# Kernel optimization log

Measured on AMD Instinct MI355X. Metric: run time of the kernel, lower is better.

## Reference

```python
import jax, jax.numpy as jnp
import numpy as np

NUM_HEADS = 8
FREQ_RATIO = 0.5


def _resize_bilinear(img, out_h, out_w):
    """Bilinear resize of last two dims, matching torch interpolate align_corners=False."""
    in_h, in_w = img.shape[-2], img.shape[-1]

    def idx(in_size, out_size):
        src = jnp.maximum((jnp.arange(out_size, dtype=jnp.float32) + 0.5) * (in_size / out_size) - 0.5, 0.0)
        i0 = jnp.floor(src).astype(jnp.int32)
        i1 = jnp.minimum(i0 + 1, in_size - 1)
        w = src - i0.astype(jnp.float32)
        return i0, i1, w

    r0, r1, wr = idx(in_h, out_h)
    img = img[..., r0, :] * (1.0 - wr)[:, None] + img[..., r1, :] * wr[:, None]
    c0, c1, wc = idx(in_w, out_w)
    img = img[..., c0] * (1.0 - wc) + img[..., c1] * wc
    return img


def setup_inputs() -> dict:
    key = jax.random.key(0)
    ks = jax.random.split(key, 6)
    B, T, J, C = 4, 256, 17, 512
    H = NUM_HEADS
    x = jax.random.normal(ks[0], (B, T, J, C), dtype=jnp.float32)
    att_map = jax.random.uniform(ks[1], (B, H, J, T, T), dtype=jnp.float32)
    weight = jax.random.uniform(ks[2], (1,), dtype=jnp.float32)
    w_qkv = jax.random.normal(ks[3], (C, 3 * C), dtype=jnp.float32) * 0.02
    w_proj = jax.random.normal(ks[4], (C, C), dtype=jnp.float32) * 0.02
    b_proj = jnp.zeros((C,), dtype=jnp.float32)
    freq_gate = jnp.ones((1,), dtype=jnp.float32)
    return {"x": x, "att_map": att_map, "weight": weight, "w_qkv": w_qkv,
            "w_proj": w_proj, "b_proj": b_proj, "freq_gate": freq_gate}


def reference(x, att_map, weight, w_qkv, w_proj, b_proj, freq_gate):
    B, T, J, C = x.shape
    H = NUM_HEADS
    d = C // H
    scale = d ** (-0.5)

    qkv = (x @ w_qkv).reshape(B, T, J, 3, H, d)
    qkv = jnp.transpose(qkv, (3, 0, 4, 2, 1, 5))  # [3,B,H,J,T,d]
    q, k, v = qkv[0], qkv[1], qkv[2]

    # time-domain attention over T, per (B,H,J)
    attn_time = jax.nn.softmax(jnp.einsum('bhjtd,bhjsd->bhjts', q, k) * scale, axis=-1)

    # frequency-domain attention
    qf = jnp.fft.rfft(q, axis=3)
    kf = jnp.fft.rfft(k, axis=3)
    F = qf.shape[3]                      # T//2 + 1
    keep = max(1, int(F * FREQ_RATIO))
    qf = qf[:, :, :, :keep]
    kf = kf[:, :, :, :keep]
    af = jnp.einsum('bhjfd,bhjgd->bhjfg', qf, jnp.conj(kf)) * scale  # complex [B,H,J,keep,keep]
    # torch combines softmax(real) + 1j*softmax(imag); only the real part survives
    af_real = jax.nn.softmax(af.real, axis=-1)
    af_real = jnp.pad(af_real, ((0, 0), (0, 0), (0, 0), (0, F - keep), (0, 0)))  # zero-pad rows to F
    attn_freq = _resize_bilinear(af_real, T, T)  # [B,H,J,T,T]

    gate = jax.nn.sigmoid(freq_gate)  # broadcastable scalar
    attn_self = gate * attn_freq + (1.0 - gate) * attn_time
    attn = weight * attn_self + (1.0 - weight) * att_map

    out = jnp.einsum('bhjts,bhjsd->bhjtd', attn, v)        # [B,H,J,T,d]
    out = jnp.transpose(out, (0, 3, 2, 1, 4)).reshape(B, T, J, C)
    return out @ w_proj + b_proj
```

## Files before the change

kernel.cpp:

```cpp
#include <hip/hip_runtime.h>
#include <hip/hip_bf16.h>


#define SCALE 0.125f
#define LSTR 72

typedef __attribute__((ext_vector_type(4))) float f32x4;
typedef __attribute__((ext_vector_type(8))) short bf16x8;
typedef __attribute__((ext_vector_type(8))) unsigned short u16x8;

__device__ __forceinline__ float bf2f(unsigned short u) {
  return __uint_as_float(((unsigned int)u) << 16);
}
__device__ __forceinline__ unsigned short f2bf(float f) {
  unsigned int u = __float_as_uint(f);
  u += 0x7FFFu + ((u >> 16) & 1u);
  return (unsigned short)(u >> 16);
}

__global__ __launch_bounds__(256) void conv_x(
    const float* __restrict__ x, unsigned short* __restrict__ xh,
    unsigned short* __restrict__ xl) {
  const size_t i = ((size_t)blockIdx.x * 256 + threadIdx.x) * 8;
  float4 a = *(const float4*)(x + i);
  float4 b = *(const float4*)(x + i + 4);
  float vv[8] = {a.x, a.y, a.z, a.w, b.x, b.y, b.z, b.w};
  u16x8 hi, lo;
#pragma unroll
  for (int e = 0; e < 8; ++e) {
    unsigned short h = f2bf(vv[e]);
    hi[e] = h;
    lo[e] = f2bf(vv[e] - bf2f(h));
  }
  *(u16x8*)&xh[i] = hi;
  *(u16x8*)&xl[i] = lo;
}

__global__ __launch_bounds__(256) void conv_wT(
    const float* __restrict__ w, unsigned short* __restrict__ th,
    unsigned short* __restrict__ tl, int N) {
  __shared__ float T[64][65];
  const int tid = threadIdx.x;
  const int nt = blockIdx.x * 64, kt = blockIdx.y * 64;
  for (int i = tid; i < 4096; i += 256) {
    const int r = i >> 6, c = i & 63;
    T[r][c] = w[(size_t)(kt + r) * N + nt + c];
  }
  __syncthreads();
  for (int i = tid; i < 4096; i += 256) {
    const int rn = i >> 6, ck = i & 63;
    const float v = T[ck][rn];
    const unsigned short h = f2bf(v);
    const size_t o = (size_t)(nt + rn) * 512 + kt + ck;
    th[o] = h;
    tl[o] = f2bf(v - bf2f(h));
  }
}

__global__ __launch_bounds__(256, 2) void qkv_gemm(
    const unsigned short* __restrict__ xh, const unsigned short* __restrict__ xl,
    const unsigned short* __restrict__ wh, const unsigned short* __restrict__ wl,
    float* __restrict__ q, float* __restrict__ k, float* __restrict__ v) {
  __shared__ __attribute__((aligned(16))) unsigned short Wt[2][128 * LSTR];
  __shared__ __attribute__((aligned(16))) unsigned short Xt[2][128 * LSTR];

  const int tid = threadIdx.x;
  const int bx = blockIdx.x, by = blockIdx.y;
  const int wid = tid >> 6, lane = tid & 63;
  const int lr = lane & 15, lg = lane >> 4;
  const int wr = wid >> 1, wc = wid & 1;
  const int srow = tid >> 3, skg = tid & 7;

  const unsigned short* xhp = xh + (size_t)(by * 128 + srow) * 512 + skg * 8;
  const unsigned short* xlp = xl + (size_t)(by * 128 + srow) * 512 + skg * 8;
  const unsigned short* whp = wh + (size_t)(bx * 128 + srow) * 512 + skg * 8;
  const unsigned short* wlp = wl + (size_t)(bx * 128 + srow) * 512 + skg * 8;

  u16x8 rxh[4], rxl[4], rwh[4], rwl[4];
  auto loadk = [&](int k0) {
#pragma unroll
    for (int it = 0; it < 4; ++it) {
      const size_t o = (size_t)(32 * it) * 512 + k0;
      rxh[it] = *(const u16x8*)(xhp + o);
      rxl[it] = *(const u16x8*)(xlp + o);
      rwh[it] = *(const u16x8*)(whp + o);
      rwl[it] = *(const u16x8*)(wlp + o);
    }
  };

  f32x4 acc[4][4];
#pragma unroll
  for (int nt = 0; nt < 4; ++nt)
#pragma unroll
    for (int mt = 0; mt < 4; ++mt) acc[nt][mt] = (f32x4){0.f, 0.f, 0.f, 0.f};

  loadk(0);
  for (int s = 0; s < 8; ++s) {
    if (s) __syncthreads();
#pragma unroll
    for (int it = 0; it < 4; ++it) {
      const int base = (srow + 32 * it) * LSTR + skg * 8;
      *(u16x8*)&Xt[0][base] = rxh[it];
      *(u16x8*)&Xt[1][base] = rxl[it];
      *(u16x8*)&Wt[0][base] = rwh[it];
      *(u16x8*)&Wt[1][base] = rwl[it];
    }
    __syncthreads();
    if (s < 7) loadk((s + 1) * 64);
#pragma unroll
    for (int kh = 0; kh < 2; ++kh) {
      const int kbase = kh * 32 + lg * 8;
      bf16x8 Ah[4], Al[4], Bh[4], Bl[4];
#pragma unroll
      for (int nt = 0; nt < 4; ++nt) {
        const int n = wr * 64 + nt * 16 + lr;
        Ah[nt] = *(bf16x8*)&Wt[0][n * LSTR + kbase];
        Al[nt] = *(bf16x8*)&Wt[1][n * LSTR + kbase];
      }
#pragma unroll
      for (int mt = 0; mt < 4; ++mt) {
        const int m = wc * 64 + mt * 16 + lr;
        Bh[mt] = *(bf16x8*)&Xt[0][m * LSTR + kbase];
        Bl[mt] = *(bf16x8*)&Xt[1][m * LSTR + kbase];
      }
#pragma unroll
      for (int nt = 0; nt < 4; ++nt)
#pragma unroll
        for (int mt = 0; mt < 4; ++mt) {
          acc[nt][mt] = __builtin_amdgcn_mfma_f32_16x16x32_bf16(Ah[nt], Bh[mt], acc[nt][mt], 0, 0, 0);
          acc[nt][mt] = __builtin_amdgcn_mfma_f32_16x16x32_bf16(Ah[nt], Bl[mt], acc[nt][mt], 0, 0, 0);
          acc[nt][mt] = __builtin_amdgcn_mfma_f32_16x16x32_bf16(Al[nt], Bh[mt], acc[nt][mt], 0, 0, 0);
        }
    }
  }

#pragma unroll
  for (int mt = 0; mt < 4; ++mt) {
    const int m = by * 128 + wc * 64 + mt * 16 + lr;
    const int jj = m % 17;
    const int bt = m / 17;
    const int t = bt & 255;
    const int b = bt >> 8;
#pragma unroll
    for (int nt = 0; nt < 4; ++nt) {
      const int c = bx * 128 + wr * 64 + nt * 16 + lg * 4;
      const int qi = c >> 9;
      const int h = (c >> 6) & 7;
      const int dd = c & 63;
      float* dst = (qi == 0) ? q : (qi == 1) ? k : v;
      *(float4*)&dst[((size_t)((b * 8 + h) * 17 + jj)) * 16384 + t * 64 + dd] =
          make_float4(acc[nt][mt][0], acc[nt][mt][1], acc[nt][mt][2], acc[nt][mt][3]);
    }
  }
}

__global__ __launch_bounds__(256) void freq_kernel(
    const float* __restrict__ qg, const float* __restrict__ kg,
    float* __restrict__ af_out) {
  __shared__ __attribute__((aligned(16))) unsigned short qT[2][64 * 256];
  __shared__ __attribute__((aligned(16))) unsigned short QF[4][64 * 64];
  __shared__ __attribute__((aligned(16))) unsigned short KF[4][64 * 64];

  const int tid = threadIdx.x;
  const int head = blockIdx.x;
  const int w = tid >> 6, lane = tid & 63;
  const int lr = lane & 15, lg = lane >> 4;
  const int f0 = w << 4;

  bf16x8 Ech[8], Ecl[8], Esh[8], Esl[8];
  {
    const int f = f0 + lr;
#pragma unroll
    for (int kb = 0; kb < 8; ++kb) {
      bf16x8 ch, cl, sh, sl;
#pragma unroll
      for (int i = 0; i < 8; ++i) {
        int t = kb * 32 + lg * 8 + i;
        int idx = (f * t) & 255;
        float s, c;
        __sincosf((float)idx * 0.02454369260617026f, &s, &c);
        unsigned short chh = f2bf(c);
        unsigned short shh = f2bf(s);
        ch[i] = (short)chh;
        cl[i] = (short)f2bf(c - bf2f(chh));
        sh[i] = (short)shh;
        sl[i] = (short)f2bf(s - bf2f(shh));
      }
      Ech[kb] = ch; Ecl[kb] = cl; Esh[kb] = sh; Esl[kb] = sl;
    }
  }

  for (int pass = 0; pass < 2; ++pass) {
    const float* src = pass ? kg : qg;
    __syncthreads();
    const float4* s4 = (const float4*)(src + head * 16384);
    for (int i = tid; i < 4096; i += 256) {
      int t = i >> 4, dq = i & 15;
      float4 v4 = s4[i];
      float vv[4] = {v4.x, v4.y, v4.z, v4.w};
#pragma unroll
      for (int c = 0; c < 4; ++c) {
        int d = dq * 4 + c;
        unsigned short hi = f2bf(vv[c]);
        unsigned short lo = f2bf(vv[c] - bf2f(hi));
        int byo = d * 512 + ((t * 2) ^ ((d & 31) << 4));
        *(unsigned short*)((char*)qT[0] + byo) = hi;
        *(unsigned short*)((char*)qT[1] + byo) = lo;
      }
    }
    __syncthreads();

    f32x4 ar[4], ai[4];
#pragma unroll
    for (int nt = 0; nt < 4; ++nt) {
      ar[nt] = (f32x4){0.f, 0.f, 0.f, 0.f};
      ai[nt] = (f32x4){0.f, 0.f, 0.f, 0.f};
    }
#pragma unroll
    for (int kb = 0; kb < 8; ++kb) {
#pragma unroll
      for (int nt = 0; nt < 4; ++nt) {
        const int d = nt * 16 + lr;
        const int byo = d * 512 + ((kb * 64 + lg * 16) ^ ((d & 31) << 4));
        bf16x8 bh = *(bf16x8*)((char*)qT[0] + byo);
        bf16x8 bl = *(bf16x8*)((char*)qT[1] + byo);
        ar[nt] = __builtin_amdgcn_mfma_f32_16x16x32_bf16(Ech[kb], bh, ar[nt], 0, 0, 0);
        ar[nt] = __builtin_amdgcn_mfma_f32_16x16x32_bf16(Ech[kb], bl, ar[nt], 0, 0, 0);
        ar[nt] = __builtin_amdgcn_mfma_f32_16x16x32_bf16(Ecl[kb], bh, ar[nt], 0, 0, 0);
        ai[nt] = __builtin_amdgcn_mfma_f32_16x16x32_bf16(Esh[kb], bh, ai[nt], 0, 0, 0);
        ai[nt] = __builtin_amdgcn_mfma_f32_16x16x32_bf16(Esh[kb], bl, ai[nt], 0, 0, 0);
        ai[nt] = __builtin_amdgcn_mfma_f32_16x16x32_bf16(Esl[kb], bh, ai[nt], 0, 0, 0);
      }
    }
    unsigned short(*DST)[64 * 64] = pass ? KF : QF;
#pragma unroll
    for (int nt = 0; nt < 4; ++nt) {
#pragma unroll
      for (int j = 0; j < 4; ++j) {
        const int f = f0 + lg * 4 + j;
        const int d = nt * 16 + lr;
        const int byo = f * 128 + ((d * 2) ^ ((f & 7) << 4));
        float vr = ar[nt][j], vi = ai[nt][j];
        unsigned short rh = f2bf(vr);
        unsigned short ih = f2bf(vi);
        *(unsigned short*)((char*)DST[0] + byo) = rh;
        *(unsigned short*)((char*)DST[1] + byo) = f2bf(vr - bf2f(rh));
        *(unsigned short*)((char*)DST[2] + byo) = ih;
        *(unsigned short*)((char*)DST[3] + byo) = f2bf(vi - bf2f(ih));
      }
    }
  }
  __syncthreads();

  f32x4 acc[4];
#pragma unroll
  for (int nt = 0; nt < 4; ++nt) acc[nt] = (f32x4){0.f, 0.f, 0.f, 0.f};
#pragma unroll
  for (int kb = 0; kb < 2; ++kb) {
    const int fA = f0 + lr;
    const int abyo = fA * 128 + ((kb * 64 + lg * 16) ^ ((fA & 7) << 4));
    bf16x8 arh = *(bf16x8*)((char*)QF[0] + abyo);
    bf16x8 arl = *(bf16x8*)((char*)QF[1] + abyo);
    bf16x8 aih = *(bf16x8*)((char*)QF[2] + abyo);
    bf16x8 ail = *(bf16x8*)((char*)QF[3] + abyo);
#pragma unroll
    for (int nt = 0; nt < 4; ++nt) {
      const int g = nt * 16 + lr;
      const int bbyo = g * 128 + ((kb * 64 + lg * 16) ^ ((g & 7) << 4));
      bf16x8 brh = *(bf16x8*)((char*)KF[0] + bbyo);
      bf16x8 brl = *(bf16x8*)((char*)KF[1] + bbyo);
      bf16x8 bih = *(bf16x8*)((char*)KF[2] + bbyo);
      bf16x8 bil = *(bf16x8*)((char*)KF[3] + bbyo);
      acc[nt] = __builtin_amdgcn_mfma_f32_16x16x32_bf16(arh, brh, acc[nt], 0, 0, 0);
      acc[nt] = __builtin_amdgcn_mfma_f32_16x16x32_bf16(arh, brl, acc[nt], 0, 0, 0);
      acc[nt] = __builtin_amdgcn_mfma_f32_16x16x32_bf16(arl, brh, acc[nt], 0, 0, 0);
      acc[nt] = __builtin_amdgcn_mfma_f32_16x16x32_bf16(aih, bih, acc[nt], 0, 0, 0);
      acc[nt] = __builtin_amdgcn_mfma_f32_16x16x32_bf16(aih, bil, acc[nt], 0, 0, 0);
      acc[nt] = __builtin_amdgcn_mfma_f32_16x16x32_bf16(ail, bih, acc[nt], 0, 0, 0);
    }
  }

  float* outh = af_out + head * 4096;
#pragma unroll
  for (int j = 0; j < 4; ++j) {
    float m = fmaxf(fmaxf(acc[0][j], acc[1][j]), fmaxf(acc[2][j], acc[3][j]));
#pragma unroll
    for (int mask = 1; mask < 16; mask <<= 1) m = fmaxf(m, __shfl_xor(m, mask));
    float e[4];
    float rs = 0.f;
#pragma unroll
    for (int nt = 0; nt < 4; ++nt) {
      e[nt] = __expf((acc[nt][j] - m) * SCALE);
      rs += e[nt];
    }
#pragma unroll
    for (int mask = 1; mask < 16; mask <<= 1) rs += __shfl_xor(rs, mask);
    const float inv = 1.0f / rs;
    const int f = f0 + lg * 4 + j;
#pragma unroll
    for (int nt = 0; nt < 4; ++nt) outh[f * 64 + nt * 16 + lr] = e[nt] * inv;
  }
}

__global__ __launch_bounds__(256) void attn_kernel(
    const float* __restrict__ qg, const float* __restrict__ kg,
    const float* __restrict__ vg, const float* __restrict__ af,
    const float* __restrict__ att_map, const float* __restrict__ weight,
    const float* __restrict__ fgate, float* __restrict__ out_perm) {
  __shared__ unsigned short Ks[256 * 64];
  __shared__ unsigned short Vt[64 * 256];
  __shared__ unsigned short afl[64 * 66];
  __shared__ unsigned short Psc[4][16 * 40];

  const int tid = threadIdx.x;
  const int t0 = blockIdx.x << 6;
  const int head = blockIdx.y;
  const int jj = head % 17;
  const int hb = head / 17;
  const int h = hb & 7;
  const int b = hb >> 3;

  const float4* ksrc = (const float4*)(kg + head * 16384);
  const float4* vsrc = (const float4*)(vg + head * 16384);
  for (int i = tid; i < 4096; i += 256) {
    int s = i >> 4, dq = i & 15;
    float4 kf = ksrc[i];
    ushort4 k4 = make_ushort4(f2bf(kf.x), f2bf(kf.y), f2bf(kf.z), f2bf(kf.w));
    int koff = s * 128 + ((dq * 8) ^ ((s & 7) << 4));
    *(ushort4*)((char*)Ks + koff) = k4;
    float4 vf = vsrc[i];
    float vv[4] = {vf.x, vf.y, vf.z, vf.w};
#pragma unroll
    for (int c = 0; c < 4; ++c) {
      int d = dq * 4 + c;
      int voff = d * 512 + ((s * 2) ^ ((d & 7) << 4));
      *(unsigned short*)((char*)Vt + voff) = f2bf(vv[c]);
    }
  }
  const float4* asrc = (const float4*)(af + head * 4096);
  for (int i = tid; i < 1024; i += 256) {
    float4 a4 = asrc[i];
    int f = i >> 4, gq = (i & 15) << 2;
    ushort4 a4b = make_ushort4(f2bf(a4.x), f2bf(a4.y), f2bf(a4.z), f2bf(a4.w));
    *(ushort4*)&afl[f * 66 + gq] = a4b;
  }
  __syncthreads();

  const int w = tid >> 6, lane = tid & 63;
  const int lr = lane & 15, lg = lane >> 4;
  const int tw = t0 + w * 16;

  bf16x8 aq[2];
  {
    const float* qrow = qg + head * 16384 + (tw + lr) * 64 + lg * 8;
#pragma unroll
    for (int kc = 0; kc < 2; ++kc) {
      float4 q0 = *(const float4*)(qrow + kc * 32);
      float4 q1 = *(const float4*)(qrow + kc * 32 + 4);
      bf16x8 a;
      a[0] = (short)f2bf(q0.x); a[1] = (short)f2bf(q0.y);
      a[2] = (short)f2bf(q0.z); a[3] = (short)f2bf(q0.w);
      a[4] = (short)f2bf(q1.x); a[5] = (short)f2bf(q1.y);
      a[6] = (short)f2bf(q1.z); a[7] = (short)f2bf(q1.w);
      aq[kc] = a;
    }
  }

  f32x4 S[16];
#pragma unroll
  for (int nt = 0; nt < 16; ++nt) {
    f32x4 accv = {0.f, 0.f, 0.f, 0.f};
#pragma unroll
    for (int kc = 0; kc < 2; ++kc) {
      int srow = nt * 16 + lr;
      int d0 = kc * 32 + lg * 8;
      int off = srow * 128 + ((d0 * 2) ^ ((srow & 7) << 4));
      bf16x8 bk = *(bf16x8*)((char*)Ks + off);
      accv = __builtin_amdgcn_mfma_f32_16x16x32_bf16(aq[kc], bk, accv, 0, 0, 0);
    }
    S[nt] = accv;
  }

  float inv[4], mrow[4];
#pragma unroll
  for (int j = 0; j < 4; ++j) {
    float m = -1e30f;
#pragma unroll
    for (int nt = 0; nt < 16; ++nt) m = fmaxf(m, S[nt][j]);
#pragma unroll
    for (int mask = 1; mask < 16; mask <<= 1) m = fmaxf(m, __shfl_xor(m, mask));
    mrow[j] = m;
  }
#pragma unroll
  for (int j = 0; j < 4; ++j) {
    float rs = 0.f;
#pragma unroll
    for (int nt = 0; nt < 16; ++nt) {
      float e = __expf((S[nt][j] - mrow[j]) * SCALE);
      S[nt][j] = e;
      rs += e;
    }
#pragma unroll
    for (int mask = 1; mask < 16; mask <<= 1) rs += __shfl_xor(rs, mask);
    inv[j] = 1.0f / rs;
  }

  {
    const float wv = weight[0];
    const float gate = 1.0f / (1.0f + __expf(-fgate[0]));
    const float* amh = att_map + (size_t)head * 65536;
#pragma unroll
    for (int j = 0; j < 4; ++j) {
      const int t = tw + lg * 4 + j;
      float srcf = fmaxf((t + 0.5f) * (129.0f / 256.0f) - 0.5f, 0.0f);
      int f0r = (int)srcf;
      float wf = srcf - (float)f0r;
      int f1r = f0r + 1;
      if (f1r > 128) f1r = 128;
      const bool v0 = (f0r < 64), v1 = (f1r < 64);
#pragma unroll
      for (int nt = 0; nt < 16; ++nt) {
        const int s = nt * 16 + lr;
        float am = amh[t * 256 + s];
        float srcg = fmaxf((s + 0.5f) * 0.25f - 0.5f, 0.0f);
        int g0 = (int)srcg;
        float wc = srcg - (float)g0;
        int g1 = g0 + 1;
        if (g1 > 63) g1 = 63;
        float fr = 0.f;
        if (v0)
          fr += (1.0f - wf) *
                (bf2f(afl[f0r * 66 + g0]) * (1.0f - wc) + bf2f(afl[f0r * 66 + g1]) * wc);
        if (v1)
          fr += wf *
                (bf2f(afl[f1r * 66 + g0]) * (1.0f - wc) + bf2f(afl[f1r * 66 + g1]) * wc);
        float pt = S[nt][j] * inv[j];
        S[nt][j] = wv * (gate * fr + (1.0f - gate) * pt) + (1.0f - wv) * am;
      }
    }
  }

  f32x4 O[4];
#pragma unroll
  for (int dt = 0; dt < 4; ++dt) O[dt] = (f32x4){0.f, 0.f, 0.f, 0.f};
  unsigned short* psc = Psc[w];
#pragma unroll
  for (int sb = 0; sb < 8; ++sb) {
#pragma unroll
    for (int half = 0; half < 2; ++half) {
      const int nt = sb * 2 + half;
#pragma unroll
      for (int j = 0; j < 4; ++j) {
        psc[(lg * 4 + j) * 40 + half * 16 + lr] = f2bf(S[nt][j]);
      }
    }
    bf16x8 pa = *(bf16x8*)&psc[lr * 40 + lg * 8];
#pragma unroll
    for (int dt = 0; dt < 4; ++dt) {
      int d = dt * 16 + lr;
      int s0 = sb * 32 + lg * 8;
      int off = d * 512 + ((s0 * 2) ^ ((d & 7) << 4));
      bf16x8 bv = *(bf16x8*)((char*)Vt + off);
      O[dt] = __builtin_amdgcn_mfma_f32_16x16x32_bf16(pa, bv, O[dt], 0, 0, 0);
    }
  }

#pragma unroll
  for (int j = 0; j < 4; ++j) {
    const int t = tw + lg * 4 + j;
    float* orow = out_perm + ((size_t)((b * 256 + t) * 17 + jj)) * 512 + h * 64;
#pragma unroll
    for (int dt = 0; dt < 4; ++dt) {
      orow[dt * 16 + lr] = O[dt][j];
    }
  }
}

__global__ __launch_bounds__(256, 2) void proj_gemm(
    const float* __restrict__ A,
    const unsigned short* __restrict__ wh, const unsigned short* __restrict__ wl,
    const float* __restrict__ bias, float* __restrict__ out) {
  __shared__ __attribute__((aligned(16))) unsigned short Wt[2][128 * LSTR];
  __shared__ __attribute__((aligned(16))) unsigned short Xt[2][128 * LSTR];

  const int tid = threadIdx.x;
  const int bx = blockIdx.x, by = blockIdx.y;
  const int wid = tid >> 6, lane = tid & 63;
  const int lr = lane & 15, lg = lane >> 4;
  const int wr = wid >> 1, wc = wid & 1;
  const int srow = tid >> 3, skg = tid & 7;

  const float* ap = A + (size_t)(by * 128 + srow) * 512 + skg * 8;
  const unsigned short* whp = wh + (size_t)(bx * 128 + srow) * 512 + skg * 8;
  const unsigned short* wlp = wl + (size_t)(bx * 128 + srow) * 512 + skg * 8;

  float4 rA[4][2];
  u16x8 rwh[4], rwl[4];
  auto loadk = [&](int k0) {
#pragma unroll
    for (int it = 0; it < 4; ++it) {
      const size_t o = (size_t)(32 * it) * 512 + k0;
      rA[it][0] = *(const float4*)(ap + o);
      rA[it][1] = *(const float4*)(ap + o + 4);
      rwh[it] = *(const u16x8*)(whp + o);
      rwl[it] = *(const u16x8*)(wlp + o);
    }
  };

  f32x4 acc[4][4];
#pragma unroll
  for (int nt = 0; nt < 4; ++nt)
#pragma unroll
    for (int mt = 0; mt < 4; ++mt) acc[nt][mt] = (f32x4){0.f, 0.f, 0.f, 0.f};

  loadk(0);
  for (int s = 0; s < 8; ++s) {
    if (s) __syncthreads();
#pragma unroll
    for (int it = 0; it < 4; ++it) {
      const int base = (srow + 32 * it) * LSTR + skg * 8;
      float vv[8] = {rA[it][0].x, rA[it][0].y, rA[it][0].z, rA[it][0].w,
                     rA[it][1].x, rA[it][1].y, rA[it][1].z, rA[it][1].w};
      u16x8 hi, lo;
#pragma unroll
      for (int e = 0; e < 8; ++e) {
        unsigned short h = f2bf(vv[e]);
        hi[e] = h;
        lo[e] = f2bf(vv[e] - bf2f(h));
      }
      *(u16x8*)&Xt[0][base] = hi;
      *(u16x8*)&Xt[1][base] = lo;
      *(u16x8*)&Wt[0][base] = rwh[it];
      *(u16x8*)&Wt[1][base] = rwl[it];
    }
    __syncthreads();
    if (s < 7) loadk((s + 1) * 64);
#pragma unroll
    for (int kh = 0; kh < 2; ++kh) {
      const int kbase = kh * 32 + lg * 8;
      bf16x8 Ah[4], Al[4], Bh[4], Bl[4];
#pragma unroll
      for (int nt = 0; nt < 4; ++nt) {
        const int n = wr * 64 + nt * 16 + lr;
        Ah[nt] = *(bf16x8*)&Wt[0][n * LSTR + kbase];
        Al[nt] = *(bf16x8*)&Wt[1][n * LSTR + kbase];
      }
#pragma unroll
      for (int mt = 0; mt < 4; ++mt) {
        const int m = wc * 64 + mt * 16 + lr;
        Bh[mt] = *(bf16x8*)&Xt[0][m * LSTR + kbase];
        Bl[mt] = *(bf16x8*)&Xt[1][m * LSTR + kbase];
      }
#pragma unroll
      for (int nt = 0; nt < 4; ++nt)
#pragma unroll
        for (int mt = 0; mt < 4; ++mt) {
          acc[nt][mt] = __builtin_amdgcn_mfma_f32_16x16x32_bf16(Ah[nt], Bh[mt], acc[nt][mt], 0, 0, 0);
          acc[nt][mt] = __builtin_amdgcn_mfma_f32_16x16x32_bf16(Ah[nt], Bl[mt], acc[nt][mt], 0, 0, 0);
          acc[nt][mt] = __builtin_amdgcn_mfma_f32_16x16x32_bf16(Al[nt], Bh[mt], acc[nt][mt], 0, 0, 0);
        }
    }
  }

#pragma unroll
  for (int mt = 0; mt < 4; ++mt) {
    const int m = by * 128 + wc * 64 + mt * 16 + lr;
#pragma unroll
    for (int nt = 0; nt < 4; ++nt) {
      const int n = bx * 128 + wr * 64 + nt * 16 + lg * 4;
      float4 bi = *(const float4*)&bias[n];
      *(float4*)&out[(size_t)m * 512 + n] =
          make_float4(acc[nt][mt][0] + bi.x, acc[nt][mt][1] + bi.y,
                      acc[nt][mt][2] + bi.z, acc[nt][mt][3] + bi.w);
    }
  }
}

extern "C" void kernel_launch(void* const* d_in, const int* in_sizes, int n_in,
                              void* d_out, int out_size, void* d_ws, size_t ws_size,
                              hipStream_t stream) {
  (void)in_sizes; (void)n_in; (void)out_size; (void)ws_size;
  const float* x = (const float*)d_in[0];
  const float* att_map = (const float*)d_in[1];
  const float* weight = (const float*)d_in[2];
  const float* w_qkv = (const float*)d_in[3];
  const float* w_proj = (const float*)d_in[4];
  const float* b_proj = (const float*)d_in[5];
  const float* fgate = (const float*)d_in[6];
  float* out = (float*)d_out;

  char* ws = (char*)d_ws;
  const size_t HB = 35651584;
  const size_t AF = 8912896;
  float* qb = (float*)(ws);
  float* kb = (float*)(ws + HB);
  float* vb = (float*)(ws + 2 * HB);
  float* af = (float*)(ws + 3 * HB);
  char* base = ws + 3 * HB + AF;
  unsigned short* xh = (unsigned short*)(base);
  unsigned short* xl = (unsigned short*)(base + 17825792);
  float* out_perm = (float*)(base);
  unsigned short* wqh = (unsigned short*)(base + 35651584);
  unsigned short* wql = (unsigned short*)(base + 35651584 + 1572864);
  unsigned short* wph = (unsigned short*)(base + 35651584 + 2 * 1572864);
  unsigned short* wpl = (unsigned short*)(base + 35651584 + 2 * 1572864 + 524288);

  conv_x<<<4352, 256, 0, stream>>>(x, xh, xl);
  conv_wT<<<dim3(24, 8), 256, 0, stream>>>(w_qkv, wqh, wql, 1536);
  conv_wT<<<dim3(8, 8), 256, 0, stream>>>(w_proj, wph, wpl, 512);
  qkv_gemm<<<dim3(12, 136), 256, 0, stream>>>(xh, xl, wqh, wql, qb, kb, vb);
  freq_kernel<<<544, 256, 0, stream>>>(qb, kb, af);
  attn_kernel<<<dim3(4, 544), 256, 0, stream>>>(qb, kb, vb, af, att_map, weight,
                                                fgate, out_perm);
  proj_gemm<<<dim3(4, 136), 256, 0, stream>>>(out_perm, wph, wpl, b_proj, out);
}
```

Baseline: 412.7 us.

## Store q/k/v as split bf16 in the GEMM epilogue and process one head per attention block

The QKV GEMM epilogue now writes q and k as hi/lo bf16 pairs and v as hi-only bf16 instead of fp32. The frequency kernel also writes its softmax output in bf16. This cuts intermediate write and read traffic and removes the repeated fp32-to-bf16 conversion in the consumers. The attention kernel now runs one block per head and loops over four 16-row tiles per wave, so K, V and the frequency map are staged into shared memory once per head instead of four times, and the next q rows are prefetched. The trade-offs are fewer blocks (544) with more serial work each, and bf16 rounding of the frequency map before it reaches global memory.

```diff
diff --git a/kernel.cpp b/kernel.cpp
--- a/kernel.cpp
+++ b/kernel.cpp
@@ -60,7 +60,9 @@
 __global__ __launch_bounds__(256, 2) void qkv_gemm(
     const unsigned short* __restrict__ xh, const unsigned short* __restrict__ xl,
     const unsigned short* __restrict__ wh, const unsigned short* __restrict__ wl,
-    float* __restrict__ q, float* __restrict__ k, float* __restrict__ v) {
+    unsigned short* __restrict__ qh, unsigned short* __restrict__ ql,
+    unsigned short* __restrict__ kh, unsigned short* __restrict__ kl,
+    unsigned short* __restrict__ vh) {
   __shared__ __attribute__((aligned(16))) unsigned short Wt[2][128 * LSTR];
   __shared__ __attribute__((aligned(16))) unsigned short Xt[2][128 * LSTR];
 
@@ -108,8 +110,8 @@
     __syncthreads();
     if (s < 7) loadk((s + 1) * 64);
 #pragma unroll
-    for (int kh = 0; kh < 2; ++kh) {
-      const int kbase = kh * 32 + lg * 8;
+    for (int kh2 = 0; kh2 < 2; ++kh2) {
+      const int kbase = kh2 * 32 + lg * 8;
       bf16x8 Ah[4], Al[4], Bh[4], Bl[4];
 #pragma unroll
       for (int nt = 0; nt < 4; ++nt) {
@@ -147,16 +149,28 @@
       const int qi = c >> 9;
       const int h = (c >> 6) & 7;
       const int dd = c & 63;
-      float* dst = (qi == 0) ? q : (qi == 1) ? k : v;
-      *(float4*)&dst[((size_t)((b * 8 + h) * 17 + jj)) * 16384 + t * 64 + dd] =
-          make_float4(acc[nt][mt][0], acc[nt][mt][1], acc[nt][mt][2], acc[nt][mt][3]);
+      const size_t base = ((size_t)((b * 8 + h) * 17 + jj)) * 16384 + t * 64 + dd;
+      float a0 = acc[nt][mt][0], a1 = acc[nt][mt][1], a2 = acc[nt][mt][2],
+            a3 = acc[nt][mt][3];
+      ushort4 hi4 = make_ushort4(f2bf(a0), f2bf(a1), f2bf(a2), f2bf(a3));
+      if (qi == 2) {
+        *(ushort4*)&vh[base] = hi4;
+      } else {
+        ushort4 lo4 = make_ushort4(f2bf(a0 - bf2f(hi4.x)), f2bf(a1 - bf2f(hi4.y)),
+                                   f2bf(a2 - bf2f(hi4.z)), f2bf(a3 - bf2f(hi4.w)));
+        unsigned short* dh = qi ? kh : qh;
+        unsigned short* dl = qi ? kl : ql;
+        *(ushort4*)&dh[base] = hi4;
+        *(ushort4*)&dl[base] = lo4;
+      }
     }
   }
 }
 
 __global__ __launch_bounds__(256) void freq_kernel(
-    const float* __restrict__ qg, const float* __restrict__ kg,
-    float* __restrict__ af_out) {
+    const unsigned short* __restrict__ qhp, const unsigned short* __restrict__ qlp,
+    const unsigned short* __restrict__ khp, const unsigned short* __restrict__ klp,
+    unsigned short* __restrict__ af_out) {
   __shared__ __attribute__((aligned(16))) unsigned short qT[2][64 * 256];
   __shared__ __attribute__((aligned(16))) unsigned short QF[4][64 * 64];
   __shared__ __attribute__((aligned(16))) unsigned short KF[4][64 * 64];
@@ -191,21 +205,21 @@
   }
 
   for (int pass = 0; pass < 2; ++pass) {
-    const float* src = pass ? kg : qg;
+    const unsigned short* sh_ = (pass ? khp : qhp) + head * 16384;
+    const unsigned short* sl_ = (pass ? klp : qlp) + head * 16384;
     __syncthreads();
-    const float4* s4 = (const float4*)(src + head * 16384);
     for (int i = tid; i < 4096; i += 256) {
       int t = i >> 4, dq = i & 15;
-      float4 v4 = s4[i];
-      float vv[4] = {v4.x, v4.y, v4.z, v4.w};
+      ushort4 hv = *(const ushort4*)&sh_[t * 64 + dq * 4];
+      ushort4 lv = *(const ushort4*)&sl_[t * 64 + dq * 4];
+      unsigned short hvv[4] = {hv.x, hv.y, hv.z, hv.w};
+      unsigned short lvv[4] = {lv.x, lv.y, lv.z, lv.w};
 #pragma unroll
       for (int c = 0; c < 4; ++c) {
         int d = dq * 4 + c;
-        unsigned short hi = f2bf(vv[c]);
-        unsigned short lo = f2bf(vv[c] - bf2f(hi));
         int byo = d * 512 + ((t * 2) ^ ((d & 31) << 4));
-        *(unsigned short*)((char*)qT[0] + byo) = hi;
-        *(unsigned short*)((char*)qT[1] + byo) = lo;
+        *(unsigned short*)((char*)qT[0] + byo) = hvv[c];
+        *(unsigned short*)((char*)qT[1] + byo) = lvv[c];
       }
     }
     __syncthreads();
@@ -280,7 +294,7 @@
     }
   }
 
-  float* outh = af_out + head * 4096;
+  unsigned short* outh = af_out + head * 4096;
 #pragma unroll
   for (int j = 0; j < 4; ++j) {
     float m = fmaxf(fmaxf(acc[0][j], acc[1][j]), fmaxf(acc[2][j], acc[3][j]));
@@ -298,13 +312,13 @@
     const float inv = 1.0f / rs;
     const int f = f0 + lg * 4 + j;
 #pragma unroll
-    for (int nt = 0; nt < 4; ++nt) outh[f * 64 + nt * 16 + lr] = e[nt] * inv;
+    for (int nt = 0; nt < 4; ++nt) outh[f * 64 + nt * 16 + lr] = f2bf(e[nt] * inv);
   }
 }
 
 __global__ __launch_bounds__(256) void attn_kernel(
-    const float* __restrict__ qg, const float* __restrict__ kg,
-    const float* __restrict__ vg, const float* __restrict__ af,
+    const unsigned short* __restrict__ qhp, const unsigned short* __restrict__ khp,
+    const unsigned short* __restrict__ vhp, const unsigned short* __restrict__ af,
     const float* __restrict__ att_map, const float* __restrict__ weight,
     const float* __restrict__ fgate, float* __restrict__ out_perm) {
   __shared__ unsigned short Ks[256 * 64];
@@ -313,102 +327,104 @@
   __shared__ unsigned short Psc[4][16 * 40];
 
   const int tid = threadIdx.x;
-  const int t0 = blockIdx.x << 6;
-  const int head = blockIdx.y;
+  const int head = blockIdx.x;
   const int jj = head % 17;
   const int hb = head / 17;
   const int h = hb & 7;
   const int b = hb >> 3;
-
-  const float4* ksrc = (const float4*)(kg + head * 16384);
-  const float4* vsrc = (const float4*)(vg + head * 16384);
+  const int w = tid >> 6, lane = tid & 63;
+  const int lr = lane & 15, lg = lane >> 4;
+
+  const float* amh = att_map + (size_t)head * 65536;
+  const unsigned short* qbase = qhp + head * 16384;
+
+  bf16x8 rq[2];
+  {
+    const unsigned short* qrow = qbase + (w * 64 + lr) * 64 + lg * 8;
+    rq[0] = *(const bf16x8*)(qrow);
+    rq[1] = *(const bf16x8*)(qrow + 32);
+  }
+
+  const unsigned short* ksrc = khp + head * 16384;
+  const unsigned short* vsrc = vhp + head * 16384;
+  for (int i = tid; i < 2048; i += 256) {
+    int s = i >> 3, dq8 = i & 7;
+    u16x8 kv = *(const u16x8*)&ksrc[s * 64 + dq8 * 8];
+    int koff = s * 128 + ((dq8 * 16) ^ ((s & 7) << 4));
+    *(u16x8*)((char*)Ks + koff) = kv;
+  }
   for (int i = tid; i < 4096; i += 256) {
     int s = i >> 4, dq = i & 15;
-    float4 kf = ksrc[i];
-    ushort4 k4 = make_ushort4(f2bf(kf.x), f2bf(kf.y), f2bf(kf.z), f2bf(kf.w));
-    int koff = s * 128 + ((dq * 8) ^ ((s & 7) << 4));
-    *(ushort4*)((char*)Ks + koff) = k4;
-    float4 vf = vsrc[i];
-    float vv[4] = {vf.x, vf.y, vf.z, vf.w};
+    ushort4 v4 = *(const ushort4*)&vsrc[s * 64 + dq * 4];
+    unsigned short vv[4] = {v4.x, v4.y, v4.z, v4.w};
 #pragma unroll
     for (int c = 0; c < 4; ++c) {
       int d = dq * 4 + c;
       int voff = d * 512 + ((s * 2) ^ ((d & 7) << 4));
-      *(unsigned short*)((char*)Vt + voff) = f2bf(vv[c]);
-    }
-  }
-  const float4* asrc = (const float4*)(af + head * 4096);
+      *(unsigned short*)((char*)Vt + voff) = vv[c];
+    }
+  }
+  const unsigned short* asrc = af + head * 4096;
   for (int i = tid; i < 1024; i += 256) {
-    float4 a4 = asrc[i];
     int f = i >> 4, gq = (i & 15) << 2;
-    ushort4 a4b = make_ushort4(f2bf(a4.x), f2bf(a4.y), f2bf(a4.z), f2bf(a4.w));
-    *(ushort4*)&afl[f * 66 + gq] = a4b;
+    *(ushort4*)&afl[f * 66 + gq] = *(const ushort4*)&asrc[f * 64 + gq];
   }
   __syncthreads();
 
-  const int w = tid >> 6, lane = tid & 63;
-  const int lr = lane & 15, lg = lane >> 4;
-  const int tw = t0 + w * 16;
-
-  bf16x8 aq[2];
-  {
-    const float* qrow = qg + head * 16384 + (tw + lr) * 64 + lg * 8;
-#pragma unroll
-    for (int kc = 0; kc < 2; ++kc) {
-      float4 q0 = *(const float4*)(qrow + kc * 32);
-      float4 q1 = *(const float4*)(qrow + kc * 32 + 4);
-      bf16x8 a;
-      a[0] = (short)f2bf(q0.x); a[1] = (short)f2bf(q0.y);
-      a[2] = (short)f2bf(q0.z); a[3] = (short)f2bf(q0.w);
-      a[4] = (short)f2bf(q1.x); a[5] = (short)f2bf(q1.y);
-      a[6] = (short)f2bf(q1.z); a[7] = (short)f2bf(q1.w);
-      aq[kc] = a;
-    }
-  }
-
-  f32x4 S[16];
-#pragma unroll
-  for (int nt = 0; nt < 16; ++nt) {
-    f32x4 accv = {0.f, 0.f, 0.f, 0.f};
-#pragma unroll
-    for (int kc = 0; kc < 2; ++kc) {
-      int srow = nt * 16 + lr;
-      int d0 = kc * 32 + lg * 8;
-      int off = srow * 128 + ((d0 * 2) ^ ((srow & 7) << 4));
-      bf16x8 bk = *(bf16x8*)((char*)Ks + off);
-      accv = __builtin_amdgcn_mfma_f32_16x16x32_bf16(aq[kc], bk, accv, 0, 0, 0);
-    }
-    S[nt] = accv;
-  }
-
-  float inv[4], mrow[4];
-#pragma unroll
-  for (int j = 0; j < 4; ++j) {
-    float m = -1e30f;
-#pragma unroll
-    for (int nt = 0; nt < 16; ++nt) m = fmaxf(m, S[nt][j]);
-#pragma unroll
-    for (int mask = 1; mask < 16; mask <<= 1) m = fmaxf(m, __shfl_xor(m, mask));
-    mrow[j] = m;
-  }
-#pragma unroll
-  for (int j = 0; j < 4; ++j) {
-    float rs = 0.f;
+  const float wv = weight[0];
+  const float gate = 1.0f / (1.0f + __expf(-fgate[0]));
+  unsigned short* psc = Psc[w];
+
+  for (int tt = 0; tt < 4; ++tt) {
+    const int tw = w * 64 + tt * 16;
+
+    bf16x8 aq[2] = {rq[0], rq[1]};
+
+    f32x4 S[16];
 #pragma unroll
     for (int nt = 0; nt < 16; ++nt) {
-      float e = __expf((S[nt][j] - mrow[j]) * SCALE);
-      S[nt][j] = e;
-      rs += e;
-    }
-#pragma unroll
-    for (int mask = 1; mask < 16; mask <<= 1) rs += __shfl_xor(rs, mask);
-    inv[j] = 1.0f / rs;
-  }
-
-  {
-    const float wv = weight[0];
-    const float gate = 1.0f / (1.0f + __expf(-fgate[0]));
-    const float* amh = att_map + (size_t)head * 65536;
+      f32x4 accv = {0.f, 0.f, 0.f, 0.f};
+#pragma unroll
+      for (int kc = 0; kc < 2; ++kc) {
+        int srow = nt * 16 + lr;
+        int d0 = kc * 32 + lg * 8;
+        int off = srow * 128 + ((d0 * 2) ^ ((srow & 7) << 4));
+        bf16x8 bk = *(bf16x8*)((char*)Ks + off);
+        accv = __builtin_amdgcn_mfma_f32_16x16x32_bf16(aq[kc], bk, accv, 0, 0, 0);
+      }
+      S[nt] = accv;
+    }
+
+    if (tt < 3) {
+      const unsigned short* qrow = qbase + (tw + 16 + lr) * 64 + lg * 8;
+      rq[0] = *(const bf16x8*)(qrow);
+      rq[1] = *(const bf16x8*)(qrow + 32);
+    }
+
+    float inv[4], mrow[4];
+#pragma unroll
+    for (int j = 0; j < 4; ++j) {
+      float m = -1e30f;
+#pragma unroll
+      for (int nt = 0; nt < 16; ++nt) m = fmaxf(m, S[nt][j]);
+#pragma unroll
+      for (int mask = 1; mask < 16; mask <<= 1) m = fmaxf(m, __shfl_xor(m, mask));
+      mrow[j] = m;
+    }
+#pragma unroll
+    for (int j = 0; j < 4; ++j) {
+      float rs = 0.f;
+#pragma unroll
+      for (int nt = 0; nt < 16; ++nt) {
+        float e = __expf((S[nt][j] - mrow[j]) * SCALE);
+        S[nt][j] = e;
+        rs += e;
+      }
+#pragma unroll
+      for (int mask = 1; mask < 16; mask <<= 1) rs += __shfl_xor(rs, mask);
+      inv[j] = 1.0f / rs;
+    }
+
 #pragma unroll
     for (int j = 0; j < 4; ++j) {
       const int t = tw + lg * 4 + j;
@@ -438,40 +454,39 @@
         S[nt][j] = wv * (gate * fr + (1.0f - gate) * pt) + (1.0f - wv) * am;
       }
     }
-  }
-
-  f32x4 O[4];
-#pragma unroll
-  for (int dt = 0; dt < 4; ++dt) O[dt] = (f32x4){0.f, 0.f, 0.f, 0.f};
-  unsigned short* psc = Psc[w];
-#pragma unroll
-  for (int sb = 0; sb < 8; ++sb) {
-#pragma unroll
-    for (int half = 0; half < 2; ++half) {
-      const int nt = sb * 2 + half;
-#pragma unroll
-      for (int j = 0; j < 4; ++j) {
-        psc[(lg * 4 + j) * 40 + half * 16 + lr] = f2bf(S[nt][j]);
-      }
-    }
-    bf16x8 pa = *(bf16x8*)&psc[lr * 40 + lg * 8];
-#pragma unroll
-    for (int dt = 0; dt < 4; ++dt) {
-      int d = dt * 16 + lr;
-      int s0 = sb * 32 + lg * 8;
-      int off = d * 512 + ((s0 * 2) ^ ((d & 7) << 4));
-      bf16x8 bv = *(bf16x8*)((char*)Vt + off);
-      O[dt] = __builtin_amdgcn_mfma_f32_16x16x32_bf16(pa, bv, O[dt], 0, 0, 0);
-    }
-  }
-
-#pragma unroll
-  for (int j = 0; j < 4; ++j) {
-    const int t = tw + lg * 4 + j;
-    float* orow = out_perm + ((size_t)((b * 256 + t) * 17 + jj)) * 512 + h * 64;
-#pragma unroll
-    for (int dt = 0; dt < 4; ++dt) {
-      orow[dt * 16 + lr] = O[dt][j];
+
+    f32x4 O[4];
+#pragma unroll
+    for (int dt = 0; dt < 4; ++dt) O[dt] = (f32x4){0.f, 0.f, 0.f, 0.f};
+#pragma unroll
+    for (int sb = 0; sb < 8; ++sb) {
+#pragma unroll
+      for (int half = 0; half < 2; ++half) {
+        const int nt = sb * 2 + half;
+#pragma unroll
+        for (int j = 0; j < 4; ++j) {
+          psc[(lg * 4 + j) * 40 + half * 16 + lr] = f2bf(S[nt][j]);
+        }
+      }
+      bf16x8 pa = *(bf16x8*)&psc[lr * 40 + lg * 8];
+#pragma unroll
+      for (int dt = 0; dt < 4; ++dt) {
+        int d = dt * 16 + lr;
+        int s0 = sb * 32 + lg * 8;
+        int off = d * 512 + ((s0 * 2) ^ ((d & 7) << 4));
+        bf16x8 bv = *(bf16x8*)((char*)Vt + off);
+        O[dt] = __builtin_amdgcn_mfma_f32_16x16x32_bf16(pa, bv, O[dt], 0, 0, 0);
+      }
+    }
+
+#pragma unroll
+    for (int j = 0; j < 4; ++j) {
+      const int t = tw + lg * 4 + j;
+      float* orow = out_perm + ((size_t)((b * 256 + t) * 17 + jj)) * 512 + h * 64;
+#pragma unroll
+      for (int dt = 0; dt < 4; ++dt) {
+        orow[dt * 16 + lr] = O[dt][j];
+      }
     }
   }
 }
@@ -536,8 +551,8 @@
     __syncthreads();
     if (s < 7) loadk((s + 1) * 64);
 #pragma unroll
-    for (int kh = 0; kh < 2; ++kh) {
-      const int kbase = kh * 32 + lg * 8;
+    for (int kh2 = 0; kh2 < 2; ++kh2) {
+      const int kbase = kh2 * 32 + lg * 8;
       bf16x8 Ah[4], Al[4], Bh[4], Bl[4];
 #pragma unroll
       for (int nt = 0; nt < 4; ++nt) {
@@ -590,15 +605,16 @@
   float* out = (float*)d_out;
 
   char* ws = (char*)d_ws;
-  const size_t HB = 35651584;
-  const size_t AF = 8912896;
-  float* qb = (float*)(ws);
-  float* kb = (float*)(ws + HB);
-  float* vb = (float*)(ws + 2 * HB);
-  float* af = (float*)(ws + 3 * HB);
-  char* base = ws + 3 * HB + AF;
+  const size_t PB = 17825792;
+  unsigned short* qh = (unsigned short*)(ws);
+  unsigned short* ql = (unsigned short*)(ws + PB);
+  unsigned short* kh = (unsigned short*)(ws + 2 * PB);
+  unsigned short* kl = (unsigned short*)(ws + 3 * PB);
+  unsigned short* vh = (unsigned short*)(ws + 4 * PB);
+  unsigned short* af = (unsigned short*)(ws + 5 * PB);
+  char* base = ws + 5 * PB + 4456448;
   unsigned short* xh = (unsigned short*)(base);
-  unsigned short* xl = (unsigned short*)(base + 17825792);
+  unsigned short* xl = (unsigned short*)(base + PB);
   float* out_perm = (float*)(base);
   unsigned short* wqh = (unsigned short*)(base + 35651584);
   unsigned short* wql = (unsigned short*)(base + 35651584 + 1572864);
@@ -608,9 +624,9 @@
   conv_x<<<4352, 256, 0, stream>>>(x, xh, xl);
   conv_wT<<<dim3(24, 8), 256, 0, stream>>>(w_qkv, wqh, wql, 1536);
   conv_wT<<<dim3(8, 8), 256, 0, stream>>>(w_proj, wph, wpl, 512);
-  qkv_gemm<<<dim3(12, 136), 256, 0, stream>>>(xh, xl, wqh, wql, qb, kb, vb);
-  freq_kernel<<<544, 256, 0, stream>>>(qb, kb, af);
-  attn_kernel<<<dim3(4, 544), 256, 0, stream>>>(qb, kb, vb, af, att_map, weight,
-                                                fgate, out_perm);
+  qkv_gemm<<<dim3(12, 136), 256, 0, stream>>>(xh, xl, wqh, wql, qh, ql, kh, kl, vh);
+  freq_kernel<<<544, 256, 0, stream>>>(qh, ql, kh, kl, af);
+  attn_kernel<<<544, 256, 0, stream>>>(qh, kh, vh, af, att_map, weight, fgate,
+                                       out_perm);
   proj_gemm<<<dim3(4, 136), 256, 0, stream>>>(out_perm, wph, wpl, b_proj, out);
 }
```

After: 396.6 us. -3.9%, faster.
